# Kernel optimization log

Measured on AMD Instinct MI355X. Metric: run time of the kernel, lower is better.

Reference implementation:

```python
import jax, jax.numpy as jnp
import numpy as np

N, E, IN_FT, OUT_FT = 20000, 4096, 128, 128


def setup_inputs() -> dict:
    key = jax.random.key(0)
    kx, kh, kw = jax.random.split(key, 3)
    X = jax.random.normal(kx, (N, IN_FT), dtype=jnp.float32)
    H = jax.random.randint(kh, (N, E), 0, 2, dtype=jnp.int32)
    weight = jax.random.normal(kw, (IN_FT, OUT_FT), dtype=jnp.float32) * (1.0 / np.sqrt(IN_FT))
    bias = jnp.zeros((OUT_FT,), dtype=jnp.float32)
    return {"X": X, "H": H, "weight": weight, "bias": bias}


def reference(X, H, weight, bias):
    # Dv^{-1/2} H De^{-1} H^T Dv^{-1/2} X W + b, with diag matrices fused as
    # row/column scalings (same math as the torch.diag @ chain, no NxN temporaries).
    Hf = H.astype(jnp.float32)
    v_deg = jnp.sum(Hf, axis=1)            # [N]
    e_deg = jnp.sum(Hf, axis=0)            # [E]
    v_deg = jnp.where(v_deg > 0, v_deg, 1.0)
    e_deg = jnp.where(e_deg > 0, e_deg, 1.0)
    dv_inv_sqrt = 1.0 / jnp.sqrt(v_deg)    # diag(Dv^-1/2)
    de_inv = 1.0 / e_deg                   # diag(De^-1)
    Y = dv_inv_sqrt[:, None] * X
    T = Hf.T @ Y                           # H^T (...)        [E, in]
    T = de_inv[:, None] * T                # De^-1 (...)
    Z = Hf @ T                             # H (...)          [N, in]
    Z = dv_inv_sqrt[:, None] * Z           # Dv^-1/2 (...)
    out = Z @ weight + bias                # [N, out]
    return out
```

## Files before the change

### kernel.cpp

```cpp
#include <hip/hip_runtime.h>

#define NV 20000
#define NE 4096
#define FT 128
#define NW_E 128
#define NW_V 625

typedef __attribute__((ext_vector_type(8))) short short8v;
typedef __attribute__((ext_vector_type(4))) float float4v;

__device__ __forceinline__ unsigned short f2bf(float f) {
    unsigned u = __float_as_uint(f);
    u += 0x7FFFu + ((u >> 16) & 1u);
    return (unsigned short)(u >> 16);
}
__device__ __forceinline__ unsigned pair_bf(unsigned w, int b) {
    return (((w >> b) & 1u) ? 0x3F80u : 0u) | (((w >> (b + 1)) & 1u) ? 0x3F800000u : 0u);
}
__device__ __forceinline__ int lds_off(int r, int chunk) {
    return r * 128 + ((chunk ^ (r & 7)) << 4);
}

__global__ __launch_bounds__(128) void k_pack(const int* __restrict__ H,
                                              unsigned* __restrict__ packed,
                                              float* __restrict__ dv) {
    int n = blockIdx.x, t = threadIdx.x;
    const uint4* row = reinterpret_cast<const uint4*>(H + (size_t)n * NE + t * 32);
    unsigned m = 0;
#pragma unroll
    for (int i = 0; i < 8; ++i) {
        uint4 v = row[i];
        m |= (v.x ? 1u : 0u) << (i * 4 + 0);
        m |= (v.y ? 1u : 0u) << (i * 4 + 1);
        m |= (v.z ? 1u : 0u) << (i * 4 + 2);
        m |= (v.w ? 1u : 0u) << (i * 4 + 3);
    }
    packed[n * NW_E + t] = m;
    int c = __popc(m);
    __shared__ int red[2];
    for (int o = 32; o > 0; o >>= 1) c += __shfl_down(c, o, 64);
    if ((t & 63) == 0) red[t >> 6] = c;
    __syncthreads();
    if (t == 0) {
        int deg = red[0] + red[1];
        dv[n] = deg > 0 ? 1.0f / sqrtf((float)deg) : 1.0f;
    }
}

__global__ __launch_bounds__(256) void k_btrans(const unsigned* __restrict__ packed,
                                                unsigned* __restrict__ packedT) {
    int lane = threadIdx.x & 63;
    int w = threadIdx.x >> 6;
    int ew = blockIdx.y * 4 + w;
    int n = blockIdx.x * 64 + lane;
    unsigned wv = (n < NV) ? packed[n * NW_E + ew] : 0u;
    unsigned my = 0;
#pragma unroll
    for (int j = 0; j < 32; ++j) {
        unsigned long long m = __ballot(((wv >> j) & 1u) != 0);
        unsigned part = (lane < 32) ? (unsigned)m : (unsigned)(m >> 32);
        if ((lane & 31) == j) my = part;
    }
    int nw = blockIdx.x * 2 + (lane >> 5);
    int e = ew * 32 + (lane & 31);
    if (nw < NW_V) packedT[e * NW_V + nw] = my;
}

__global__ __launch_bounds__(64) void k_edeg(const unsigned* __restrict__ packedT,
                                             float* __restrict__ de) {
    int e = blockIdx.x, l = threadIdx.x;
    const unsigned* row = packedT + e * NW_V;
    int c = 0;
    for (int i = l; i < NW_V; i += 64) c += __popc(row[i]);
    for (int o = 32; o > 0; o >>= 1) c += __shfl_down(c, o, 64);
    if (l == 0) de[e] = c > 0 ? 1.0f / (float)c : 1.0f;
}

__global__ __launch_bounds__(256) void k_ybft(const float* __restrict__ X,
                                              const float* __restrict__ dv,
                                              unsigned short* __restrict__ Ybf) {
    int t = threadIdx.x;
    int f = t & 127;
    int nb = (blockIdx.x * 2 + (t >> 7)) * 8;
    unsigned short h[8];
#pragma unroll
    for (int i = 0; i < 8; ++i) {
        float v = X[(size_t)(nb + i) * FT + f] * dv[nb + i];
        h[i] = f2bf(v);
    }
    uint4 u;
    u.x = (unsigned)h[0] | ((unsigned)h[1] << 16);
    u.y = (unsigned)h[2] | ((unsigned)h[3] << 16);
    u.z = (unsigned)h[4] | ((unsigned)h[5] << 16);
    u.w = (unsigned)h[6] | ((unsigned)h[7] << 16);
    *reinterpret_cast<uint4*>(Ybf + (size_t)f * NV + nb) = u;
}

__global__ __launch_bounds__(256, 2) void k_mm1(const unsigned short* __restrict__ Ybf,
                                                const unsigned* __restrict__ packedT,
                                                float* __restrict__ P, int chunkK) {
    __shared__ __align__(16) unsigned char sA[128 * 128];
    __shared__ __align__(16) unsigned char sB[128 * 128];
    int t = threadIdx.x;
    int et = blockIdx.x & 31, kp = blockIdx.x >> 5;
    int e0 = et * 128;
    int kbeg = kp * chunkK;
    int iters = chunkK >> 6;

    float4v acc[4][4];
#pragma unroll
    for (int i = 0; i < 4; ++i)
#pragma unroll
        for (int j = 0; j < 4; ++j)
#pragma unroll
            for (int r = 0; r < 4; ++r) acc[i][j][r] = 0.0f;

    int fA = t & 127;
    int chbA = (t >> 7) * 4;
    const unsigned short* arow = Ybf + (size_t)fA * NV;
    int eB = t & 127;
    int hB = t >> 7;
    const unsigned* brow = packedT + (size_t)(e0 + eB) * NW_V;

    int wave = t >> 6, lane = t & 63;
    int wm0 = (wave & 1) * 64, wc0 = (wave >> 1) * 64;
    int r0 = lane & 15, q = lane >> 4;

    for (int it = 0; it < iters; ++it) {
        int k0 = kbeg + it * 64;
#pragma unroll
        for (int c = 0; c < 4; ++c) {
            int ch = chbA + c;
            int n = k0 + ch * 8;
            uint4 v = {0, 0, 0, 0};
            if (n < NV) v = *reinterpret_cast<const uint4*>(arow + n);
            *reinterpret_cast<uint4*>(sA + lds_off(fA, ch)) = v;
        }
        {
            int nw = (k0 >> 5) + hB;
            unsigned wv = (nw < NW_V) ? brow[nw] : 0u;
#pragma unroll
            for (int c = 0; c < 4; ++c) {
                int b0 = c * 8;
                uint4 u;
                u.x = pair_bf(wv, b0);     u.y = pair_bf(wv, b0 + 2);
                u.z = pair_bf(wv, b0 + 4); u.w = pair_bf(wv, b0 + 6);
                *reinterpret_cast<uint4*>(sB + lds_off(eB, hB * 4 + c)) = u;
            }
        }
        __syncthreads();
#pragma unroll
        for (int ks = 0; ks < 2; ++ks) {
            short8v a[4], b[4];
#pragma unroll
            for (int mi = 0; mi < 4; ++mi)
                a[mi] = *reinterpret_cast<const short8v*>(sA + lds_off(wm0 + mi * 16 + r0, ks * 4 + q));
#pragma unroll
            for (int ci = 0; ci < 4; ++ci)
                b[ci] = *reinterpret_cast<const short8v*>(sB + lds_off(wc0 + ci * 16 + r0, ks * 4 + q));
#pragma unroll
            for (int mi = 0; mi < 4; ++mi)
#pragma unroll
                for (int ci = 0; ci < 4; ++ci)
                    acc[mi][ci] = __builtin_amdgcn_mfma_f32_16x16x32_bf16(a[mi], b[ci], acc[mi][ci], 0, 0, 0);
        }
        __syncthreads();
    }
    float* Pp = P + (size_t)kp * (128 * 4096);
#pragma unroll
    for (int mi = 0; mi < 4; ++mi)
#pragma unroll
        for (int ci = 0; ci < 4; ++ci) {
            int f = wm0 + mi * 16 + q * 4;
            int e = e0 + wc0 + ci * 16 + r0;
#pragma unroll
            for (int r = 0; r < 4; ++r)
                Pp[(size_t)(f + r) * 4096 + e] = acc[mi][ci][r];
        }
}

__global__ __launch_bounds__(256) void k_reduce(const float4v* __restrict__ P,
                                                float4v* __restrict__ Tt, int S) {
    int i = blockIdx.x * 256 + threadIdx.x;
    float4v a = P[i];
    for (int p = 1; p < S; ++p) a += P[(size_t)p * 131072 + i];
    Tt[i] = a;
}

__global__ __launch_bounds__(256) void k_ut(const float* __restrict__ Tt,
                                            const float* __restrict__ W,
                                            const float* __restrict__ de,
                                            unsigned short* __restrict__ Ubf) {
    int t = threadIdx.x;
    int e = blockIdx.x * 64 + (t & 63);
    int g0 = blockIdx.y * 16 + (t >> 6) * 4;
    float a0 = 0, a1 = 0, a2 = 0, a3 = 0;
    for (int f = 0; f < 128; ++f) {
        float tv = Tt[(size_t)f * 4096 + e];
        float4 wv = *reinterpret_cast<const float4*>(W + f * 128 + g0);
        a0 += tv * wv.x; a1 += tv * wv.y; a2 += tv * wv.z; a3 += tv * wv.w;
    }
    float d = de[e];
    Ubf[(size_t)(g0 + 0) * 4096 + e] = f2bf(a0 * d);
    Ubf[(size_t)(g0 + 1) * 4096 + e] = f2bf(a1 * d);
    Ubf[(size_t)(g0 + 2) * 4096 + e] = f2bf(a2 * d);
    Ubf[(size_t)(g0 + 3) * 4096 + e] = f2bf(a3 * d);
}

__global__ __launch_bounds__(256, 2) void k_mm2(const unsigned* __restrict__ packed,
                                                const unsigned short* __restrict__ Ubf,
                                                const float* __restrict__ dv,
                                                const float* __restrict__ bias,
                                                float* __restrict__ out) {
    __shared__ __align__(16) unsigned char sA[128 * 128];
    __shared__ __align__(16) unsigned char sB[64 * 128];
    int t = threadIdx.x;
    int mt = blockIdx.x >> 1, half = blockIdx.x & 1;
    int n0 = mt * 128, g0 = half * 64;

    float4v acc[4][2];
#pragma unroll
    for (int i = 0; i < 4; ++i)
#pragma unroll
        for (int j = 0; j < 2; ++j)
#pragma unroll
            for (int r = 0; r < 4; ++r) acc[i][j][r] = 0.0f;

    int nA = t & 127, hA = t >> 7;
    int gB = t & 63, chbB = (t >> 6) * 2;
    const unsigned short* brow = Ubf + (size_t)(g0 + gB) * 4096;

    int wave = t >> 6, lane = t & 63;
    int wm0 = (wave & 1) * 64, wc0 = (wave >> 1) * 32;
    int r0 = lane & 15, q = lane >> 4;

    for (int k0 = 0; k0 < 4096; k0 += 64) {
        {
            unsigned wv = (n0 + nA < NV) ? packed[(size_t)(n0 + nA) * NW_E + (k0 >> 5) + hA] : 0u;
#pragma unroll
            for (int c = 0; c < 4; ++c) {
                int b0 = c * 8;
                uint4 u;
                u.x = pair_bf(wv, b0);     u.y = pair_bf(wv, b0 + 2);
                u.z = pair_bf(wv, b0 + 4); u.w = pair_bf(wv, b0 + 6);
                *reinterpret_cast<uint4*>(sA + lds_off(nA, hA * 4 + c)) = u;
            }
        }
#pragma unroll
        for (int c = 0; c < 2; ++c) {
            int ch = chbB + c;
            uint4 v = *reinterpret_cast<const uint4*>(brow + k0 + ch * 8);
            *reinterpret_cast<uint4*>(sB + lds_off(gB, ch)) = v;
        }
        __syncthreads();
#pragma unroll
        for (int ks = 0; ks < 2; ++ks) {
            short8v a[4], b[2];
#pragma unroll
            for (int mi = 0; mi < 4; ++mi)
                a[mi] = *reinterpret_cast<const short8v*>(sA + lds_off(wm0 + mi * 16 + r0, ks * 4 + q));
#pragma unroll
            for (int ci = 0; ci < 2; ++ci)
                b[ci] = *reinterpret_cast<const short8v*>(sB + lds_off(wc0 + ci * 16 + r0, ks * 4 + q));
#pragma unroll
            for (int mi = 0; mi < 4; ++mi)
#pragma unroll
                for (int ci = 0; ci < 2; ++ci)
                    acc[mi][ci] = __builtin_amdgcn_mfma_f32_16x16x32_bf16(a[mi], b[ci], acc[mi][ci], 0, 0, 0);
        }
        __syncthreads();
    }
#pragma unroll
    for (int ci = 0; ci < 2; ++ci) {
        int g = g0 + wc0 + ci * 16 + r0;
        float bg = bias[g];
#pragma unroll
        for (int mi = 0; mi < 4; ++mi) {
#pragma unroll
            for (int r = 0; r < 4; ++r) {
                int n = n0 + wm0 + mi * 16 + q * 4 + r;
                if (n < NV) out[(size_t)n * 128 + g] = dv[n] * acc[mi][ci][r] + bg;
            }
        }
    }
}

extern "C" void kernel_launch(void* const* d_in, const int* in_sizes, int n_in,
                              void* d_out, int out_size, void* d_ws, size_t ws_size,
                              hipStream_t stream) {
    const float* X    = (const float*)d_in[0];
    const int*   H    = (const int*)d_in[1];
    const float* W    = (const float*)d_in[2];
    const float* bias = (const float*)d_in[3];
    float* out = (float*)d_out;

    char* ws = (char*)d_ws;
    size_t off = 0;
    auto alloc = [&](size_t sz) { char* p = ws + off; off += (sz + 255) & ~(size_t)255; return p; };
    unsigned*       packed  = (unsigned*)alloc((size_t)NV * NW_E * 4);
    unsigned*       packedT = (unsigned*)alloc((size_t)NE * NW_V * 4);
    unsigned short* Ybf     = (unsigned short*)alloc((size_t)FT * NV * 2);
    float*          Tt      = (float*)alloc((size_t)FT * NE * 4);
    unsigned short* Ubf     = (unsigned short*)alloc((size_t)FT * NE * 2);
    float*          dv      = (float*)alloc((size_t)NV * 4);
    float*          de      = (float*)alloc((size_t)NE * 4);
    size_t fixed = off;

    long long avail = (long long)ws_size - (long long)fixed;
    int S = (int)(avail / (128LL * 4096 * 4));
    if (S > 16) S = 16;
    if (S < 1) S = 1;
    float* P1 = (float*)(ws + fixed);
    int chunkK = ((NV + S * 64 - 1) / (S * 64)) * 64;

    k_pack  <<<NV, 128, 0, stream>>>(H, packed, dv);
    k_btrans<<<dim3(313, 32), 256, 0, stream>>>(packed, packedT);
    k_edeg  <<<NE, 64, 0, stream>>>(packedT, de);
    k_ybft  <<<1250, 256, 0, stream>>>(X, dv, Ybf);
    k_mm1   <<<32 * S, 256, 0, stream>>>(Ybf, packedT, P1, chunkK);
    k_reduce<<<512, 256, 0, stream>>>((const float4v*)P1, (float4v*)Tt, S);
    k_ut    <<<dim3(64, 8), 256, 0, stream>>>(Tt, W, de, Ubf);
    k_mm2   <<<314, 256, 0, stream>>>(packed, Ubf, dv, bias, out);
}
```

Baseline: 621.4 us.

## Fuse H bit-packing with transpose and degree partials; use LDS LUT for bf16 expansion

After: 628.6 us. No clear change (+1.2%).

```diff
diff --git a/kernel.cpp b/kernel.cpp
--- a/kernel.cpp
+++ b/kernel.cpp
@@ -5,6 +5,7 @@
 #define FT 128
 #define NW_E 128
 #define NW_V 625
+#define NVP 20032
 
 typedef __attribute__((ext_vector_type(8))) short short8v;
 typedef __attribute__((ext_vector_type(4))) float float4v;
@@ -14,66 +15,85 @@
     u += 0x7FFFu + ((u >> 16) & 1u);
     return (unsigned short)(u >> 16);
 }
-__device__ __forceinline__ unsigned pair_bf(unsigned w, int b) {
-    return (((w >> b) & 1u) ? 0x3F80u : 0u) | (((w >> (b + 1)) & 1u) ? 0x3F800000u : 0u);
-}
 __device__ __forceinline__ int lds_off(int r, int chunk) {
     return r * 128 + ((chunk ^ (r & 7)) << 4);
 }
-
-__global__ __launch_bounds__(128) void k_pack(const int* __restrict__ H,
-                                              unsigned* __restrict__ packed,
-                                              float* __restrict__ dv) {
-    int n = blockIdx.x, t = threadIdx.x;
-    const uint4* row = reinterpret_cast<const uint4*>(H + (size_t)n * NE + t * 32);
-    unsigned m = 0;
-#pragma unroll
-    for (int i = 0; i < 8; ++i) {
-        uint4 v = row[i];
-        m |= (v.x ? 1u : 0u) << (i * 4 + 0);
-        m |= (v.y ? 1u : 0u) << (i * 4 + 1);
-        m |= (v.z ? 1u : 0u) << (i * 4 + 2);
-        m |= (v.w ? 1u : 0u) << (i * 4 + 3);
-    }
-    packed[n * NW_E + t] = m;
-    int c = __popc(m);
-    __shared__ int red[2];
-    for (int o = 32; o > 0; o >>= 1) c += __shfl_down(c, o, 64);
-    if ((t & 63) == 0) red[t >> 6] = c;
+__device__ __forceinline__ uint4 lut_entry(int t) {
+    uint4 e;
+    e.x = ((t & 1) ? 0x3F80u : 0u) | ((t & 2) ? 0x3F800000u : 0u);
+    e.y = ((t & 4) ? 0x3F80u : 0u) | ((t & 8) ? 0x3F800000u : 0u);
+    e.z = ((t & 16) ? 0x3F80u : 0u) | ((t & 32) ? 0x3F800000u : 0u);
+    e.w = ((t & 64) ? 0x3F80u : 0u) | ((t & 128) ? 0x3F800000u : 0u);
+    return e;
+}
+
+__global__ __launch_bounds__(256) void k_packt(const int* __restrict__ H,
+                                               unsigned* __restrict__ packed,
+                                               unsigned* __restrict__ packedT,
+                                               int* __restrict__ dvp) {
+    __shared__ int cl[64];
+    int b = blockIdx.x;
+    int g = b >> 1, h = b & 1;
+    int t = threadIdx.x, lane = t & 63;
+    int w0 = h * 64 + (t >> 6) * 16;
+    int n = g * 64 + lane;
+    bool valid = n < NV;
+    const uint4* base = reinterpret_cast<const uint4*>(H) + (size_t)n * (NE / 4);
+
+    if (t < 64) cl[t] = 0;
     __syncthreads();
-    if (t == 0) {
-        int deg = red[0] + red[1];
-        dv[n] = deg > 0 ? 1.0f / sqrtf((float)deg) : 1.0f;
-    }
-}
-
-__global__ __launch_bounds__(256) void k_btrans(const unsigned* __restrict__ packed,
-                                                unsigned* __restrict__ packedT) {
-    int lane = threadIdx.x & 63;
-    int w = threadIdx.x >> 6;
-    int ew = blockIdx.y * 4 + w;
-    int n = blockIdx.x * 64 + lane;
-    unsigned wv = (n < NV) ? packed[n * NW_E + ew] : 0u;
-    unsigned my = 0;
-#pragma unroll
-    for (int j = 0; j < 32; ++j) {
-        unsigned long long m = __ballot(((wv >> j) & 1u) != 0);
-        unsigned part = (lane < 32) ? (unsigned)m : (unsigned)(m >> 32);
-        if ((lane & 31) == j) my = part;
-    }
-    int nw = blockIdx.x * 2 + (lane >> 5);
-    int e = ew * 32 + (lane & 31);
-    if (nw < NW_V) packedT[e * NW_V + nw] = my;
-}
-
-__global__ __launch_bounds__(64) void k_edeg(const unsigned* __restrict__ packedT,
-                                             float* __restrict__ de) {
-    int e = blockIdx.x, l = threadIdx.x;
-    const unsigned* row = packedT + e * NW_V;
-    int c = 0;
-    for (int i = l; i < NW_V; i += 64) c += __popc(row[i]);
-    for (int o = 32; o > 0; o >>= 1) c += __shfl_down(c, o, 64);
-    if (l == 0) de[e] = c > 0 ? 1.0f / (float)c : 1.0f;
+
+    int cnt = 0;
+    int nw = g * 2 + (lane >> 5);
+    for (int it = 0; it < 16; ++it) {
+        int w = w0 + it;
+        unsigned m = 0;
+        if (valid) {
+            const uint4* p = base + w * 8;
+#pragma unroll
+            for (int i = 0; i < 8; ++i) {
+                uint4 v = p[i];
+                m |= (v.x ? 1u : 0u) << (i * 4 + 0);
+                m |= (v.y ? 1u : 0u) << (i * 4 + 1);
+                m |= (v.z ? 1u : 0u) << (i * 4 + 2);
+                m |= (v.w ? 1u : 0u) << (i * 4 + 3);
+            }
+            packed[(size_t)n * NW_E + w] = m;
+        }
+        cnt += __popc(m);
+        unsigned my = 0;
+#pragma unroll
+        for (int j = 0; j < 32; ++j) {
+            unsigned long long bm = __ballot(((m >> j) & 1u) != 0);
+            unsigned part = (lane < 32) ? (unsigned)bm : (unsigned)(bm >> 32);
+            if ((lane & 31) == j) my = part;
+        }
+        int e = w * 32 + (lane & 31);
+        if (nw < NW_V) packedT[(size_t)e * NW_V + nw] = my;
+    }
+    atomicAdd(&cl[lane], cnt);
+    __syncthreads();
+    if (t < 64) dvp[h * NVP + g * 64 + t] = cl[t];
+}
+
+__global__ __launch_bounds__(64) void k_deg(const unsigned* __restrict__ packedT,
+                                            const int* __restrict__ dvp,
+                                            float* __restrict__ de,
+                                            float* __restrict__ dv) {
+    int bid = blockIdx.x, l = threadIdx.x;
+    if (bid < NE) {
+        const unsigned* row = packedT + (size_t)bid * NW_V;
+        int c = 0;
+        for (int i = l; i < NW_V; i += 64) c += __popc(row[i]);
+        for (int o = 32; o > 0; o >>= 1) c += __shfl_down(c, o, 64);
+        if (l == 0) de[bid] = c > 0 ? 1.0f / (float)c : 1.0f;
+    } else {
+        int i = (bid - NE) * 64 + l;
+        if (i < NV) {
+            int d = dvp[i] + dvp[NVP + i];
+            dv[i] = d > 0 ? 1.0f / sqrtf((float)d) : 1.0f;
+        }
+    }
 }
 
 __global__ __launch_bounds__(256) void k_ybft(const float* __restrict__ X,
@@ -101,7 +121,11 @@
                                                 float* __restrict__ P, int chunkK) {
     __shared__ __align__(16) unsigned char sA[128 * 128];
     __shared__ __align__(16) unsigned char sB[128 * 128];
+    __shared__ __align__(16) uint4 slut[256];
     int t = threadIdx.x;
+    slut[t] = lut_entry(t & 255);
+    if (t < 256 - 256) {}
+
     int et = blockIdx.x & 31, kp = blockIdx.x >> 5;
     int e0 = et * 128;
     int kbeg = kp * chunkK;
@@ -125,6 +149,7 @@
     int wave = t >> 6, lane = t & 63;
     int wm0 = (wave & 1) * 64, wc0 = (wave >> 1) * 64;
     int r0 = lane & 15, q = lane >> 4;
+    __syncthreads();
 
     for (int it = 0; it < iters; ++it) {
         int k0 = kbeg + it * 64;
@@ -141,28 +166,25 @@
             unsigned wv = (nw < NW_V) ? brow[nw] : 0u;
 #pragma unroll
             for (int c = 0; c < 4; ++c) {
-                int b0 = c * 8;
-                uint4 u;
-                u.x = pair_bf(wv, b0);     u.y = pair_bf(wv, b0 + 2);
-                u.z = pair_bf(wv, b0 + 4); u.w = pair_bf(wv, b0 + 6);
+                uint4 u = slut[(wv >> (c * 8)) & 0xFF];
                 *reinterpret_cast<uint4*>(sB + lds_off(eB, hB * 4 + c)) = u;
             }
         }
         __syncthreads();
 #pragma unroll
         for (int ks = 0; ks < 2; ++ks) {
-            short8v a[4], b[4];
+            short8v a[4], bb[4];
 #pragma unroll
             for (int mi = 0; mi < 4; ++mi)
                 a[mi] = *reinterpret_cast<const short8v*>(sA + lds_off(wm0 + mi * 16 + r0, ks * 4 + q));
 #pragma unroll
             for (int ci = 0; ci < 4; ++ci)
-                b[ci] = *reinterpret_cast<const short8v*>(sB + lds_off(wc0 + ci * 16 + r0, ks * 4 + q));
+                bb[ci] = *reinterpret_cast<const short8v*>(sB + lds_off(wc0 + ci * 16 + r0, ks * 4 + q));
 #pragma unroll
             for (int mi = 0; mi < 4; ++mi)
 #pragma unroll
                 for (int ci = 0; ci < 4; ++ci)
-                    acc[mi][ci] = __builtin_amdgcn_mfma_f32_16x16x32_bf16(a[mi], b[ci], acc[mi][ci], 0, 0, 0);
+                    acc[mi][ci] = __builtin_amdgcn_mfma_f32_16x16x32_bf16(a[mi], bb[ci], acc[mi][ci], 0, 0, 0);
         }
         __syncthreads();
     }
@@ -214,7 +236,10 @@
                                                 float* __restrict__ out) {
     __shared__ __align__(16) unsigned char sA[128 * 128];
     __shared__ __align__(16) unsigned char sB[64 * 128];
+    __shared__ __align__(16) uint4 slut[256];
     int t = threadIdx.x;
+    slut[t] = lut_entry(t & 255);
+
     int mt = blockIdx.x >> 1, half = blockIdx.x & 1;
     int n0 = mt * 128, g0 = half * 64;
 
@@ -233,16 +258,14 @@
     int wave = t >> 6, lane = t & 63;
     int wm0 = (wave & 1) * 64, wc0 = (wave >> 1) * 32;
     int r0 = lane & 15, q = lane >> 4;
+    __syncthreads();
 
     for (int k0 = 0; k0 < 4096; k0 += 64) {
         {
             unsigned wv = (n0 + nA < NV) ? packed[(size_t)(n0 + nA) * NW_E + (k0 >> 5) + hA] : 0u;
 #pragma unroll
             for (int c = 0; c < 4; ++c) {
-                int b0 = c * 8;
-                uint4 u;
-                u.x = pair_bf(wv, b0);     u.y = pair_bf(wv, b0 + 2);
-                u.z = pair_bf(wv, b0 + 4); u.w = pair_bf(wv, b0 + 6);
+                uint4 u = slut[(wv >> (c * 8)) & 0xFF];
                 *reinterpret_cast<uint4*>(sA + lds_off(nA, hA * 4 + c)) = u;
             }
         }
@@ -255,18 +278,18 @@
         __syncthreads();
 #pragma unroll
         for (int ks = 0; ks < 2; ++ks) {
-            short8v a[4], b[2];
+            short8v a[4], bb[2];
 #pragma unroll
             for (int mi = 0; mi < 4; ++mi)
                 a[mi] = *reinterpret_cast<const short8v*>(sA + lds_off(wm0 + mi * 16 + r0, ks * 4 + q));
 #pragma unroll
             for (int ci = 0; ci < 2; ++ci)
-                b[ci] = *reinterpret_cast<const short8v*>(sB + lds_off(wc0 + ci * 16 + r0, ks * 4 + q));
+                bb[ci] = *reinterpret_cast<const short8v*>(sB + lds_off(wc0 + ci * 16 + r0, ks * 4 + q));
 #pragma unroll
             for (int mi = 0; mi < 4; ++mi)
 #pragma unroll
                 for (int ci = 0; ci < 2; ++ci)
-                    acc[mi][ci] = __builtin_amdgcn_mfma_f32_16x16x32_bf16(a[mi], b[ci], acc[mi][ci], 0, 0, 0);
+                    acc[mi][ci] = __builtin_amdgcn_mfma_f32_16x16x32_bf16(a[mi], bb[ci], acc[mi][ci], 0, 0, 0);
         }
         __syncthreads();
     }
@@ -304,6 +327,7 @@
     unsigned short* Ubf     = (unsigned short*)alloc((size_t)FT * NE * 2);
     float*          dv      = (float*)alloc((size_t)NV * 4);
     float*          de      = (float*)alloc((size_t)NE * 4);
+    int*            dvp     = (int*)alloc((size_t)2 * NVP * 4);
     size_t fixed = off;
 
     long long avail = (long long)ws_size - (long long)fixed;
@@ -313,9 +337,8 @@
     float* P1 = (float*)(ws + fixed);
     int chunkK = ((NV + S * 64 - 1) / (S * 64)) * 64;
 
-    k_pack  <<<NV, 128, 0, stream>>>(H, packed, dv);
-    k_btrans<<<dim3(313, 32), 256, 0, stream>>>(packed, packedT);
-    k_edeg  <<<NE, 64, 0, stream>>>(packedT, de);
+    k_packt <<<626, 256, 0, stream>>>(H, packed, packedT, dvp);
+    k_deg   <<<NE + 313, 64, 0, stream>>>(packedT, dvp, de, dv);
     k_ybft  <<<1250, 256, 0, stream>>>(X, dv, Ybf);
     k_mm1   <<<32 * S, 256, 0, stream>>>(Ybf, packedT, P1, chunkK);
     k_reduce<<<512, 256, 0, stream>>>((const float4v*)P1, (float4v*)Tt, S);
```
